# Optimization experiments

Hardware: AMD Instinct MI355X
Metric: run time of the kernel (lower is better)

The kernel has to match this reference:

```python
import jax, jax.numpy as jnp
import numpy as np

# hyperparams from speculative_config
MIN_N, MAX_N, K = 3, 5, 8
B, S, TOKEN_RANGE = 512, 8192, 32


def setup_inputs() -> dict:
    key = jax.random.key(0)
    k1, k2, k3 = jax.random.split(key, 3)
    token_ids_gpu = jax.random.randint(k1, (B, S), 0, TOKEN_RANGE, dtype=jnp.int32)
    num_tokens_no_spec = jax.random.randint(k2, (B,), 0, S, dtype=jnp.int32)
    combined_mask = jax.random.bernoulli(k3, 0.9, (B,))
    return {
        "num_tokens_no_spec": num_tokens_no_spec,
        "token_ids_gpu": token_ids_gpu,
        "combined_mask": combined_mask,
    }


def _find_first_and_extract(data, seq_lengths, min_n, max_n, result_len):
    """Parallel multi-length n-gram match; returns [B, result_len]."""
    bsz, max_seq_len = data.shape
    num_windows = max_seq_len - max_n + 1
    # all sliding windows of length max_n: [B, num_windows, max_n]
    win_idx = jnp.arange(num_windows)[:, None] + jnp.arange(max_n)[None, :]
    all_windows = data[:, win_idx]
    window_starts = jnp.arange(num_windows)

    all_first_matches = []  # per pattern length, [B]
    for n in range(min_n, max_n + 1):  # small fixed unrolled loop
        offset = max_n - n
        # trailing n tokens of each sequence = the search pattern
        pat_idx = jnp.clip((seq_lengths - n)[:, None] + jnp.arange(n)[None, :], 0, None)
        patterns = jnp.take_along_axis(data, pat_idx, axis=1)  # [B, n]
        # suffix of each max_n-window has the length-n candidate
        matches = jnp.all(all_windows[..., offset:] == patterns[:, None, :], axis=-1)
        max_valid_start = seq_lengths - n - result_len  # [B]
        pat_start_pos = window_starts + offset
        final_matches = matches & (pat_start_pos[None, :] <= max_valid_start[:, None])
        prefix_pos = jnp.arange(offset)
        if offset > 0:
            # windows starting at positions [0, offset) not covered by unfold suffixes
            gidx = jnp.clip(prefix_pos[:, None] + jnp.arange(n)[None, :], 0, max_seq_len - 1)
            prefix_tokens = data[:, gidx]  # [B, offset, n]
            prefix_matches = jnp.all(prefix_tokens == patterns[:, None, :], axis=-1)
            prefix_final = prefix_matches & (prefix_pos[None, :] <= max_valid_start[:, None])
            combined = jnp.concatenate([prefix_final, final_matches], axis=1)
            start_positions = jnp.concatenate([prefix_pos, pat_start_pos])
        else:
            combined = final_matches
            start_positions = pat_start_pos
        first_idx = jnp.argmax(combined, axis=1)  # first True (or 0 if none)
        has_match = jnp.take_along_axis(combined, first_idx[:, None], axis=1)[:, 0]
        match_pos = start_positions[first_idx]
        all_first_matches.append(jnp.where(has_match, match_pos, -1))

    afm = jnp.stack(all_first_matches, axis=1)  # [B, num_patterns]
    num_patterns = max_n - min_n + 1
    best_idx = num_patterns - 1 - jnp.argmax(jnp.flip(afm >= 0, axis=1), axis=1)
    best_pos = jnp.take_along_axis(afm, best_idx[:, None], axis=1)[:, 0]
    has_any = best_pos >= 0
    best_len = jnp.arange(min_n, max_n + 1)[best_idx]
    result_starts = jnp.where(has_any, best_pos + best_len, 0)
    ridx = jnp.clip(result_starts[:, None] + jnp.arange(result_len), 0, max_seq_len - 1)
    extracted = jnp.take_along_axis(data, ridx, axis=1)
    return jnp.where(has_any[:, None], extracted, jnp.zeros_like(extracted))


def reference(num_tokens_no_spec, token_ids_gpu, combined_mask):
    results = _find_first_and_extract(token_ids_gpu, num_tokens_no_spec, MIN_N, MAX_N, K)
    draft = jnp.where(combined_mask[:, None], results, jnp.zeros_like(results))
    return draft.astype(jnp.int32)
```

## Files before the change

kernel.cpp:

```cpp
#include <hip/hip_runtime.h>
#include <limits.h>

#define BATCH 512
#define SEQ   8192
#define KLEN  8

__global__ __launch_bounds__(1024)
void ngram_match_kernel(const int* __restrict__ num_tokens,
                        const int* __restrict__ tokens,
                        const int* __restrict__ mask,
                        int* __restrict__ out)
{
    const int b   = blockIdx.x;
    const int tid = threadIdx.x;
    const int L   = num_tokens[b];
    const long base = (long)b * SEQ;

    __shared__ int s_min[3];
    __shared__ int s_start;
    if (tid < 3) s_min[tid] = INT_MAX;
    __syncthreads();

    const int limit3 = L - 3 - KLEN;
    const int limit4 = L - 4 - KLEN;
    const int limit5 = L - 5 - KLEN;

    int pat0 = 0, pat1 = 0, pat2 = 0, pat3 = 0, pat4 = 0;
    if (limit3 >= 0) {
        pat2 = tokens[base + L - 3];
        pat3 = tokens[base + L - 2];
        pat4 = tokens[base + L - 1];
        if (limit4 >= 0) pat1 = tokens[base + L - 4];
        if (limit5 >= 0) pat0 = tokens[base + L - 5];
    }

    int m3 = INT_MAX, m4 = INT_MAX, m5 = INT_MAX;

    for (int p0 = tid * 4; p0 <= limit3; p0 += (int)blockDim.x * 4) {
        const int4 va = *(const int4*)(tokens + base + p0);
        const int4 vb = *(const int4*)(tokens + base + p0 + 4);
        int w[8] = { va.x, va.y, va.z, va.w, vb.x, vb.y, vb.z, vb.w };
        #pragma unroll
        for (int j = 0; j < 4; ++j) {
            const int p = p0 + j;
            const bool q3 = (w[j]   == pat2) & (w[j+1] == pat3) & (w[j+2] == pat4)
                            & (p <= limit3);
            const bool q4 = (w[j]   == pat1) & (w[j+1] == pat2) & (w[j+2] == pat3)
                            & (w[j+3] == pat4) & (p <= limit4);
            const bool q5 = (w[j]   == pat0) & (w[j+1] == pat1) & (w[j+2] == pat2)
                            & (w[j+3] == pat3) & (w[j+4] == pat4) & (p <= limit5);
            if (q3) m3 = min(m3, p);
            if (q4) m4 = min(m4, p);
            if (q5) m5 = min(m5, p);
        }
    }

    if (m3 != INT_MAX) atomicMin(&s_min[0], m3);
    if (m4 != INT_MAX) atomicMin(&s_min[1], m4);
    if (m5 != INT_MAX) atomicMin(&s_min[2], m5);
    __syncthreads();

    if (tid == 0) {
        int start = -1;
        if      (s_min[2] != INT_MAX) start = s_min[2] + 5;
        else if (s_min[1] != INT_MAX) start = s_min[1] + 4;
        else if (s_min[0] != INT_MAX) start = s_min[0] + 3;
        s_start = start;
    }
    __syncthreads();

    if (tid < KLEN) {
        const int start = s_start;
        int v = 0;
        if (start >= 0 && mask[b] != 0) v = tokens[base + start + tid];
        out[b * KLEN + tid] = v;
    }
}

extern "C" void kernel_launch(void* const* d_in, const int* in_sizes, int n_in,
                              void* d_out, int out_size, void* d_ws, size_t ws_size,
                              hipStream_t stream) {
    const int* num_tokens = (const int*)d_in[0];
    const int* token_ids  = (const int*)d_in[1];
    const int* cmask      = (const int*)d_in[2];
    int* out              = (int*)d_out;

    ngram_match_kernel<<<BATCH, 1024, 0, stream>>>(num_tokens, token_ids, cmask, out);
}
```

Baseline: 68.98 us.

## Split n-gram scan across sequence chunks with global atomic key and separate extract kernel

Replaces the one-block-per-batch-row kernel with a 2D grid where each 256-thread block scans a 1024-position chunk of a row. It also packs pattern length and position into a single key, so one global atomicMin yields the longest-then-earliest match. A memset and a second small kernel then decode the key and gather the draft tokens. This is meant to increase parallelism and skip blocks beyond each row's valid length, at the cost of an extra memset, a second launch and global atomics.

```diff
diff --git a/kernel.cpp b/kernel.cpp
--- a/kernel.cpp
+++ b/kernel.cpp
@@ -4,42 +4,33 @@
 #define BATCH 512
 #define SEQ   8192
 #define KLEN  8
+#define KEY_LIMIT (3 * SEQ)
 
-__global__ __launch_bounds__(1024)
-void ngram_match_kernel(const int* __restrict__ num_tokens,
-                        const int* __restrict__ tokens,
-                        const int* __restrict__ mask,
-                        int* __restrict__ out)
+__global__ __launch_bounds__(256)
+void ngram_scan(const int* __restrict__ num_tokens,
+                const int* __restrict__ tokens,
+                int* __restrict__ best)
 {
-    const int b   = blockIdx.x;
-    const int tid = threadIdx.x;
-    const int L   = num_tokens[b];
-    const long base = (long)b * SEQ;
-
-    __shared__ int s_min[3];
-    __shared__ int s_start;
-    if (tid < 3) s_min[tid] = INT_MAX;
-    __syncthreads();
-
+    const int b = blockIdx.y;
+    const int L = num_tokens[b];
     const int limit3 = L - 3 - KLEN;
     const int limit4 = L - 4 - KLEN;
     const int limit5 = L - 5 - KLEN;
+    const int p_begin = blockIdx.x * 1024;
+    if (p_begin > limit3) return;
+    const long base = (long)b * SEQ;
+    const int pat0 = tokens[base + L - 5];
+    const int pat1 = tokens[base + L - 4];
+    const int pat2 = tokens[base + L - 3];
+    const int pat3 = tokens[base + L - 2];
+    const int pat4 = tokens[base + L - 1];
 
-    int pat0 = 0, pat1 = 0, pat2 = 0, pat3 = 0, pat4 = 0;
-    if (limit3 >= 0) {
-        pat2 = tokens[base + L - 3];
-        pat3 = tokens[base + L - 2];
-        pat4 = tokens[base + L - 1];
-        if (limit4 >= 0) pat1 = tokens[base + L - 4];
-        if (limit5 >= 0) pat0 = tokens[base + L - 5];
-    }
-
-    int m3 = INT_MAX, m4 = INT_MAX, m5 = INT_MAX;
-
-    for (int p0 = tid * 4; p0 <= limit3; p0 += (int)blockDim.x * 4) {
+    int bestLocal = INT_MAX;
+    const int p0 = p_begin + (int)threadIdx.x * 4;
+    if (p0 <= limit3) {
         const int4 va = *(const int4*)(tokens + base + p0);
         const int4 vb = *(const int4*)(tokens + base + p0 + 4);
-        int w[8] = { va.x, va.y, va.z, va.w, vb.x, vb.y, vb.z, vb.w };
+        const int w[8] = { va.x, va.y, va.z, va.w, vb.x, vb.y, vb.z, vb.w };
         #pragma unroll
         for (int j = 0; j < 4; ++j) {
             const int p = p0 + j;
@@ -49,32 +40,31 @@
                             & (w[j+3] == pat4) & (p <= limit4);
             const bool q5 = (w[j]   == pat0) & (w[j+1] == pat1) & (w[j+2] == pat2)
                             & (w[j+3] == pat3) & (w[j+4] == pat4) & (p <= limit5);
-            if (q3) m3 = min(m3, p);
-            if (q4) m4 = min(m4, p);
-            if (q5) m5 = min(m5, p);
+            if (q3) bestLocal = min(bestLocal, 2 * SEQ + p);
+            if (q4) bestLocal = min(bestLocal, 1 * SEQ + p);
+            if (q5) bestLocal = min(bestLocal, p);
         }
     }
+    if (bestLocal != INT_MAX) atomicMin(&best[b], bestLocal);
+}
 
-    if (m3 != INT_MAX) atomicMin(&s_min[0], m3);
-    if (m4 != INT_MAX) atomicMin(&s_min[1], m4);
-    if (m5 != INT_MAX) atomicMin(&s_min[2], m5);
-    __syncthreads();
-
-    if (tid == 0) {
-        int start = -1;
-        if      (s_min[2] != INT_MAX) start = s_min[2] + 5;
-        else if (s_min[1] != INT_MAX) start = s_min[1] + 4;
-        else if (s_min[0] != INT_MAX) start = s_min[0] + 3;
-        s_start = start;
+__global__ __launch_bounds__(256)
+void ngram_extract(const int* __restrict__ tokens,
+                   const int* __restrict__ mask,
+                   const int* __restrict__ best,
+                   int* __restrict__ out)
+{
+    const int t = blockIdx.x * 256 + (int)threadIdx.x;
+    const int b = t >> 3;
+    const int k = t & 7;
+    const int key = best[b];
+    int v = 0;
+    if (key < KEY_LIMIT && mask[b] != 0) {
+        const int n = 5 - (key >> 13);
+        const int p = key & (SEQ - 1);
+        v = tokens[(long)b * SEQ + p + n + k];
     }
-    __syncthreads();
-
-    if (tid < KLEN) {
-        const int start = s_start;
-        int v = 0;
-        if (start >= 0 && mask[b] != 0) v = tokens[base + start + tid];
-        out[b * KLEN + tid] = v;
-    }
+    out[t] = v;
 }
 
 extern "C" void kernel_launch(void* const* d_in, const int* in_sizes, int n_in,
@@ -84,6 +74,13 @@
     const int* token_ids  = (const int*)d_in[1];
     const int* cmask      = (const int*)d_in[2];
     int* out              = (int*)d_out;
+    int* best             = (int*)d_ws;
 
-    ngram_match_kernel<<<BATCH, 1024, 0, stream>>>(num_tokens, token_ids, cmask, out);
+    hipMemsetAsync(best, 0x7F, BATCH * sizeof(int), stream);
+
+    dim3 grid_scan(SEQ / 1024, BATCH);
+    ngram_scan<<<grid_scan, 256, 0, stream>>>(num_tokens, token_ids, best);
+
+    ngram_extract<<<(BATCH * KLEN) / 256, 256, 0, stream>>>(token_ids, cmask,
+                                                            best, out);
 }
```

Result: slower. 72.02 us (+4.4%).
